# Kernel tuning notes

Measured on AMD Instinct MI355X. Metric: run time of the kernel, lower is better.

The kernel has to match this reference:

```python
import jax, jax.numpy as jnp
import numpy as np

B, NC, NT = 16, 2048, 2048
IN_DIM, H_DIM, OUT_DIM = 128, 256, 256


def _mlp(x, w1, b1, w2, b2, w3, b3):
    # MLP(input_dim, [h, h], output_dim): Linear-ReLU-Linear-ReLU-Linear
    h = jax.nn.relu(x @ w1 + b1)
    h = jax.nn.relu(h @ w2 + b2)
    return h @ w3 + b3


def setup_inputs() -> dict:
    key = jax.random.key(0)
    ks = jax.random.split(key, 16)

    def lin(k, fan_in, fan_out):
        s = 1.0 / np.sqrt(fan_in)
        kw, kb = jax.random.split(k)
        w = jax.random.uniform(kw, (fan_in, fan_out), jnp.float32, -s, s)
        b = jax.random.uniform(kb, (fan_out,), jnp.float32, -s, s)
        return w, b

    qw1, qb1 = lin(ks[0], IN_DIM, H_DIM)
    qw2, qb2 = lin(ks[1], H_DIM, H_DIM)
    qw3, qb3 = lin(ks[2], H_DIM, OUT_DIM)
    kw1, kb1 = lin(ks[3], IN_DIM, H_DIM)
    kw2, kb2 = lin(ks[4], H_DIM, H_DIM)
    kw3, kb3 = lin(ks[5], H_DIM, OUT_DIM)

    return {
        "x_context": jax.random.normal(ks[6], (B, NC, IN_DIM), jnp.float32),
        "x_target": jax.random.normal(ks[7], (B, NT, IN_DIM), jnp.float32),
        "r_i": jax.random.normal(ks[8], (B, NC, OUT_DIM), jnp.float32),
        "qw1": qw1, "qb1": qb1, "qw2": qw2, "qb2": qb2, "qw3": qw3, "qb3": qb3,
        "kw1": kw1, "kb1": kb1, "kw2": kw2, "kb2": kb2, "kw3": kw3, "kb3": kb3,
    }


def reference(x_context, x_target, r_i,
              qw1, qb1, qw2, qb2, qw3, qb3,
              kw1, kb1, kw2, kb2, kw3, kb3):
    q = _mlp(x_target, qw1, qb1, qw2, qb2, qw3, qb3)   # [B, NT, D]
    k = _mlp(x_context, kw1, kb1, kw2, kb2, kw3, kb3)  # [B, NC, D]
    scale = jnp.sqrt(jnp.asarray(k.shape[-1], dtype=jnp.float32))
    w = jnp.einsum('btd,bcd->btc', q, k) / scale       # [B, NT, NC]
    # Faithful to torch.softmax(w, dim=1): normalize over the TARGET axis.
    w = jax.nn.softmax(w, axis=1)
    return jnp.einsum('btc,bcd->btd', w, r_i)          # [B, NT, OUT_DIM]
```

## Files before the change

### kernel.cpp

```cpp
#include <hip/hip_runtime.h>

#define BB 16
#define NT 2048
#define NC 2048
#define DIM 256
#define INDIM 128

typedef unsigned short u16;
typedef __bf16 bfx8 __attribute__((ext_vector_type(8)));
typedef __bf16 bfx8a __attribute__((ext_vector_type(8), aligned(8)));
typedef float f32x4 __attribute__((ext_vector_type(4)));

__device__ __forceinline__ u16 f2bf(float f) {
    union { float f; unsigned u; } v; v.f = f;
    return (u16)((v.u + 0x7FFFu + ((v.u >> 16) & 1u)) >> 16);
}

#define MFMA16(a, b, c) __builtin_amdgcn_mfma_f32_16x16x32_bf16((a), (b), (c), 0, 0, 0)


__global__ void cvt_w_all(const float* __restrict__ w0, const float* __restrict__ w1,
                          const float* __restrict__ w2, const float* __restrict__ w3,
                          const float* __restrict__ w4, const float* __restrict__ w5,
                          u16* __restrict__ o0, u16* __restrict__ o1, u16* __restrict__ o2,
                          u16* __restrict__ o3, u16* __restrict__ o4, u16* __restrict__ o5) {
    int bx = blockIdx.x;
    const float* src; u16* dst; int K, base;
    if (bx < 128)       { src = w0; dst = o0; K = 128; base = 0; }
    else if (bx < 384)  { src = w1; dst = o1; K = 256; base = 128; }
    else if (bx < 640)  { src = w2; dst = o2; K = 256; base = 384; }
    else if (bx < 768)  { src = w3; dst = o3; K = 128; base = 640; }
    else if (bx < 1024) { src = w4; dst = o4; K = 256; base = 768; }
    else                { src = w5; dst = o5; K = 256; base = 1024; }
    int idx = (bx - base) * 256 + threadIdx.x;
    int n = idx / K, k = idx - n * K;
    dst[idx] = f2bf(src[k * 256 + n]);
}

__global__ void cvt_rt_kernel(const float* __restrict__ r, u16* __restrict__ rt) {
    __shared__ u16 tile[32][33];
    int b = blockIdx.z;
    int c0 = blockIdx.x * 32, d0 = blockIdx.y * 32;
    int tx = threadIdx.x, ty = threadIdx.y;
    const float* rb = r + (size_t)b * NC * DIM;
#pragma unroll
    for (int i = 0; i < 4; i++) {
        int c = c0 + ty + i * 8;
        tile[ty + i * 8][tx] = f2bf(rb[(size_t)c * DIM + d0 + tx]);
    }
    __syncthreads();
    u16* rtb = rt + (size_t)b * DIM * NC;
#pragma unroll
    for (int i = 0; i < 4; i++) {
        int d = d0 + ty + i * 8;
        rtb[(size_t)d * NC + c0 + tx] = tile[tx][ty + i * 8];
    }
}


__global__ __launch_bounds__(256) void mlp_fused(const float* __restrict__ xq, const float* __restrict__ xk,
                                                 const u16* __restrict__ W1q, const u16* __restrict__ W1k,
                                                 const float* __restrict__ b1q, const float* __restrict__ b1k,
                                                 const u16* __restrict__ W2q, const u16* __restrict__ W2k,
                                                 const float* __restrict__ b2q, const float* __restrict__ b2k,
                                                 const u16* __restrict__ W3q, const u16* __restrict__ W3k,
                                                 const float* __restrict__ b3q, const float* __restrict__ b3k,
                                                 u16* __restrict__ oq, u16* __restrict__ ok) {
    __shared__ __align__(16) char lds[65536];
    char* h1 = lds;
    char* xa = lds + 32768;
    char* h2 = lds + 32768;

    int tid = threadIdx.x, lane = tid & 63, w = tid >> 6;
    int lr = lane & 15, lg = lane >> 4;
    int m0 = blockIdx.x * 64;
    bool isq = (blockIdx.y == 0);
    const float* X = (isq ? xq : xk) + (size_t)m0 * INDIM;
    const u16* W1 = isq ? W1q : W1k;  const float* b1 = isq ? b1q : b1k;
    const u16* W2 = isq ? W2q : W2k;  const float* b2 = isq ? b2q : b2k;
    const u16* W3 = isq ? W3q : W3k;  const float* b3 = isq ? b3q : b3k;
    u16* C = (isq ? oq : ok) + (size_t)m0 * 256;

#pragma unroll
    for (int j = 0; j < 4; j++) {
        int bo = (j * 256 + tid) * 16;
        int row = bo >> 8;
        int ir = bo & 255;
        const float* src = X + (size_t)row * INDIM + (ir >> 1);
        float4 f0 = *reinterpret_cast<const float4*>(src);
        float4 f1 = *reinterpret_cast<const float4*>(src + 4);
        union { u16 u[8]; uint4 v; } pk;
        {
            __bf16 h;
            h = (__bf16)f0.x; pk.u[0] = *(u16*)&h;
            h = (__bf16)f0.y; pk.u[1] = *(u16*)&h;
            h = (__bf16)f0.z; pk.u[2] = *(u16*)&h;
            h = (__bf16)f0.w; pk.u[3] = *(u16*)&h;
            h = (__bf16)f1.x; pk.u[4] = *(u16*)&h;
            h = (__bf16)f1.y; pk.u[5] = *(u16*)&h;
            h = (__bf16)f1.z; pk.u[6] = *(u16*)&h;
            h = (__bf16)f1.w; pk.u[7] = *(u16*)&h;
        }
        *reinterpret_cast<uint4*>(xa + row * 256 + (ir ^ ((row & 7) << 4))) = pk.v;
    }
    __syncthreads();

    int n0 = w * 64;
    const int key = (lr & 7) << 4;

    {
        f32x4 acc[4][4] = {};
#pragma unroll
        for (int ks = 0; ks < 4; ks++) {
            bfx8 b[4];
#pragma unroll
            for (int nt = 0; nt < 4; nt++)
                b[nt] = *reinterpret_cast<const bfx8*>(W1 + (size_t)(n0 + nt * 16 + lr) * 128 + ks * 32 + lg * 8);
#pragma unroll
            for (int mt = 0; mt < 4; mt++) {
                bfx8 a = *reinterpret_cast<const bfx8*>(xa + (mt * 16 + lr) * 256 + ((ks * 64 + lg * 16) ^ key));
#pragma unroll
                for (int nt = 0; nt < 4; nt++)
                    acc[mt][nt] = MFMA16(a, b[nt], acc[mt][nt]);
            }
        }
#pragma unroll
        for (int nt = 0; nt < 4; nt++) {
            int col = n0 + nt * 16 + lr;
            float bv = b1[col];
#pragma unroll
            for (int mt = 0; mt < 4; mt++) {
#pragma unroll
                for (int r = 0; r < 4; r++) {
                    int row = mt * 16 + lg * 4 + r;
                    float v = fmaxf(acc[mt][nt][r] + bv, 0.0f);
                    *(u16*)(h1 + row * 512 + ((col * 2) ^ ((row & 7) << 4))) = f2bf(v);
                }
            }
        }
    }
    __syncthreads();

    {
        f32x4 acc[4][4] = {};
#pragma unroll
        for (int ks = 0; ks < 8; ks++) {
            bfx8 b[4];
#pragma unroll
            for (int nt = 0; nt < 4; nt++)
                b[nt] = *reinterpret_cast<const bfx8*>(W2 + (size_t)(n0 + nt * 16 + lr) * 256 + ks * 32 + lg * 8);
#pragma unroll
            for (int mt = 0; mt < 4; mt++) {
                bfx8 a = *reinterpret_cast<const bfx8*>(h1 + (mt * 16 + lr) * 512 + ((ks * 64 + lg * 16) ^ key));
#pragma unroll
                for (int nt = 0; nt < 4; nt++)
                    acc[mt][nt] = MFMA16(a, b[nt], acc[mt][nt]);
            }
        }
#pragma unroll
        for (int nt = 0; nt < 4; nt++) {
            int col = n0 + nt * 16 + lr;
            float bv = b2[col];
#pragma unroll
            for (int mt = 0; mt < 4; mt++) {
#pragma unroll
                for (int r = 0; r < 4; r++) {
                    int row = mt * 16 + lg * 4 + r;
                    float v = fmaxf(acc[mt][nt][r] + bv, 0.0f);
                    *(u16*)(h2 + row * 512 + ((col * 2) ^ ((row & 7) << 4))) = f2bf(v);
                }
            }
        }
    }
    __syncthreads();

    {
        f32x4 acc[4][4] = {};
#pragma unroll
        for (int ks = 0; ks < 8; ks++) {
            bfx8 b[4];
#pragma unroll
            for (int nt = 0; nt < 4; nt++)
                b[nt] = *reinterpret_cast<const bfx8*>(W3 + (size_t)(n0 + nt * 16 + lr) * 256 + ks * 32 + lg * 8);
#pragma unroll
            for (int mt = 0; mt < 4; mt++) {
                bfx8 a = *reinterpret_cast<const bfx8*>(h2 + (mt * 16 + lr) * 512 + ((ks * 64 + lg * 16) ^ key));
#pragma unroll
                for (int nt = 0; nt < 4; nt++)
                    acc[mt][nt] = MFMA16(a, b[nt], acc[mt][nt]);
            }
        }
#pragma unroll
        for (int nt = 0; nt < 4; nt++) {
            int col = n0 + nt * 16 + lr;
            float bv = b3[col];
#pragma unroll
            for (int mt = 0; mt < 4; mt++) {
#pragma unroll
                for (int r = 0; r < 4; r++) {
                    int row = mt * 16 + lg * 4 + r;
                    C[(size_t)row * 256 + col] = f2bf(acc[mt][nt][r] + bv);
                }
            }
        }
    }
}


__global__ __launch_bounds__(256) void stats_kernel(const u16* __restrict__ q,
                                                    const u16* __restrict__ k,
                                                    float2* __restrict__ gso) {
    int flat = blockIdx.x;
    int sw = (flat & 7) * 64 + (flat >> 3);
    int b = sw >> 5;
    int c0 = (sw & 31) * 64;
    int tid = threadIdx.x, lane = tid & 63, w = tid >> 6;
    int lr = lane & 15, lg = lane >> 4;
    const u16* qb = q + (size_t)b * NT * DIM;
    const u16* kb = k + (size_t)b * NC * DIM;
    const float A2 = 1.44269504f / 16.0f;

    bfx8 kf[4][8];
#pragma unroll
    for (int j = 0; j < 4; j++)
#pragma unroll
        for (int ks = 0; ks < 8; ks++)
            kf[j][ks] = *reinterpret_cast<const bfx8*>(kb + (size_t)(c0 + j * 16 + lr) * DIM + ks * 32 + lg * 8);

    float m_run[4], l_run[4];
#pragma unroll
    for (int j = 0; j < 4; j++) { m_run[j] = -1e30f; l_run[j] = 0.0f; }

    for (int ts = 0; ts < NT / 64; ts++) {
        int t0 = ts * 64 + w * 16;
        f32x4 acc[4] = {};
#pragma unroll
        for (int ks = 0; ks < 8; ks++) {
            bfx8 a = *reinterpret_cast<const bfx8*>(qb + (size_t)(t0 + lr) * DIM + ks * 32 + lg * 8);
#pragma unroll
            for (int j = 0; j < 4; j++)
                acc[j] = MFMA16(a, kf[j][ks], acc[j]);
        }
#pragma unroll
        for (int j = 0; j < 4; j++) {
            f32x4 a = acc[j];
            float mx = fmaxf(fmaxf(a[0], a[1]), fmaxf(a[2], a[3]));
            float mn = fmaxf(m_run[j], mx);
            float t = mn * A2;
            float sum = exp2f(fmaf(a[0], A2, -t)) + exp2f(fmaf(a[1], A2, -t)) +
                        exp2f(fmaf(a[2], A2, -t)) + exp2f(fmaf(a[3], A2, -t));
            l_run[j] = l_run[j] * exp2f(fmaf(m_run[j], A2, -t)) + sum;
            m_run[j] = mn;
        }
    }

#pragma unroll
    for (int j = 0; j < 4; j++) {
        float m = m_run[j], l = l_run[j];
#pragma unroll
        for (int d = 16; d < 64; d <<= 1) {
            float mo = __shfl_xor(m, d);
            float lo = __shfl_xor(l, d);
            float mn = fmaxf(m, mo);
            l = l * exp2f((m - mn) * A2) + lo * exp2f((mo - mn) * A2);
            m = mn;
        }
        m_run[j] = m; l_run[j] = l;
    }

    __shared__ float sm[4][64], sl[4][64];
    if (lg == 0) {
#pragma unroll
        for (int j = 0; j < 4; j++) {
            sm[w][j * 16 + lr] = m_run[j];
            sl[w][j * 16 + lr] = l_run[j];
        }
    }
    __syncthreads();
    if (tid < 64) {
        float mf = sm[0][tid];
#pragma unroll
        for (int ww = 1; ww < 4; ww++) mf = fmaxf(mf, sm[ww][tid]);
        float lf = 0.0f;
#pragma unroll
        for (int ww = 0; ww < 4; ww++) lf += sl[ww][tid] * exp2f((sm[ww][tid] - mf) * A2);
        gso[(size_t)b * NC + c0 + tid] = make_float2(mf * A2, 1.0f / lf);
    }
}


__global__ __launch_bounds__(256, 2) void attn_kernel(const u16* __restrict__ q,
                                                      const u16* __restrict__ k,
                                                      const u16* __restrict__ rt,
                                                      const float2* __restrict__ gsg_,
                                                      float* __restrict__ out) {
    int flat = blockIdx.x;
    int sw = (flat & 7) * 64 + (flat >> 3);
    int b = sw >> 5;
    int t0 = (sw & 31) * 64;
    int tid = threadIdx.x, lane = tid & 63, w = tid >> 6;
    int lr = lane & 15, lg = lane >> 4;
    const u16* qb = q + (size_t)b * NT * DIM;
    const u16* kb = k + (size_t)b * NC * DIM;
    const u16* rtb = rt + (size_t)b * DIM * NC;

    __shared__ float2 gs[NC];
    __shared__ __align__(16) u16 kt[2][32 * 256];
    __shared__ u16 pl[64][36];

    {
        const float2* gsg = gsg_ + (size_t)b * NC;
        for (int i = tid; i < NC; i += 256) gs[i] = gsg[i];
    }
    __syncthreads();

#define STAGE(nb, cc) do {                                                          \
    const u16* ksrc_ = kb + (size_t)(cc) * DIM;                                     \
    _Pragma("unroll")                                                               \
    for (int i_ = 0; i_ < 4; i_++) {                                                \
        int off_ = ((w * 4 + i_) << 10) + (lane << 4);                              \
        int row_ = off_ >> 9;                                                       \
        int ss_  = ((off_ >> 4) & 31) ^ (row_ & 7);                                 \
        const u16* g_ = ksrc_ + row_ * DIM + ss_ * 8;                               \
        __builtin_amdgcn_global_load_lds(                                           \
            (const __attribute__((address_space(1))) void*)g_,                      \
            (__attribute__((address_space(3))) void*)(&kt[nb][(w * 4 + i_) << 9]),  \
            16, 0, 0);                                                              \
    }                                                                               \
} while (0)

    STAGE(0, 0);
    __builtin_amdgcn_sched_barrier(0);
    bfx8 rb_c[4], rb_n[4];
#pragma unroll
    for (int nt = 0; nt < 4; nt++)
        rb_c[nt] = *reinterpret_cast<const bfx8*>(rtb + (size_t)(w * 64 + nt * 16 + lr) * NC + lg * 8);
    bfx8 aq[8];
#pragma unroll
    for (int ks = 0; ks < 8; ks++)
        aq[ks] = *reinterpret_cast<const bfx8*>(qb + (size_t)(t0 + w * 16 + lr) * DIM + ks * 32 + lg * 8);
    __builtin_amdgcn_sched_barrier(0);
    asm volatile("s_waitcnt vmcnt(12)");
    __builtin_amdgcn_s_barrier();
    __builtin_amdgcn_sched_barrier(0);

    const float A = 1.44269504f / 16.0f;
    const int key = lr & 7;
    f32x4 acc[4][4] = {};
    int cur = 0;

    for (int c0 = 0; c0 < NC; c0 += 32) {
        const bool last = (c0 + 32 >= NC);
        if (!last) STAGE(cur ^ 1, c0 + 32);
        __builtin_amdgcn_sched_barrier(0);
        if (!last) {
#pragma unroll
            for (int nt = 0; nt < 4; nt++)
                rb_n[nt] = *reinterpret_cast<const bfx8*>(rtb + (size_t)(w * 64 + nt * 16 + lr) * NC + (c0 + 32) + lg * 8);
        }

        f32x4 s[2] = {};
        {
            const char* kc = (const char*)&kt[cur][0];
#pragma unroll
            for (int ks = 0; ks < 8; ks++) {
                int slot = (ks << 2) | lg;
                bfx8 k0 = *reinterpret_cast<const bfx8*>(kc + (lr << 9) + (((slot ^ key)) << 4));
                bfx8 k1 = *reinterpret_cast<const bfx8*>(kc + ((16 + lr) << 9) + (((slot ^ key)) << 4));
                s[0] = MFMA16(aq[ks], k0, s[0]);
                s[1] = MFMA16(aq[ks], k1, s[1]);
            }
        }
#pragma unroll
        for (int j = 0; j < 2; j++) {
            float2 g = gs[c0 + j * 16 + lr];
#pragma unroll
            for (int r = 0; r < 4; r++) {
                float p = exp2f(fmaf(s[j][r], A, -g.x)) * g.y;
                __bf16 h = (__bf16)p;
                pl[w * 16 + lg * 4 + r][j * 16 + lr] = *(u16*)&h;
            }
        }
        __builtin_amdgcn_sched_barrier(0);
        asm volatile("s_waitcnt lgkmcnt(0)");
        __builtin_amdgcn_s_barrier();
        __builtin_amdgcn_sched_barrier(0);

#pragma unroll
        for (int mt = 0; mt < 4; mt++) {
            bfx8a pa = *reinterpret_cast<const bfx8a*>((const char*)pl + (mt * 16 + lr) * 72 + lg * 16);
#pragma unroll
            for (int nt = 0; nt < 4; nt++)
                acc[mt][nt] = MFMA16((bfx8)pa, rb_c[nt], acc[mt][nt]);
        }

        __builtin_amdgcn_sched_barrier(0);
        asm volatile("s_waitcnt vmcnt(4) lgkmcnt(0)");
        __builtin_amdgcn_s_barrier();
        __builtin_amdgcn_sched_barrier(0);

#pragma unroll
        for (int nt = 0; nt < 4; nt++) rb_c[nt] = rb_n[nt];
        cur ^= 1;
    }
#undef STAGE

    float* ob = out + (size_t)b * NT * DIM;
#pragma unroll
    for (int nt = 0; nt < 4; nt++) {
        int col = w * 64 + nt * 16 + lr;
#pragma unroll
        for (int mt = 0; mt < 4; mt++) {
            int rowb = t0 + mt * 16 + lg * 4;
#pragma unroll
            for (int r = 0; r < 4; r++)
                ob[(size_t)(rowb + r) * DIM + col] = acc[mt][nt][r];
        }
    }
}


extern "C" void kernel_launch(void* const* d_in, const int* in_sizes, int n_in,
                              void* d_out, int out_size, void* d_ws, size_t ws_size,
                              hipStream_t stream) {
    const float* xc  = (const float*)d_in[0];
    const float* xt  = (const float*)d_in[1];
    const float* ri  = (const float*)d_in[2];
    const float* qw1 = (const float*)d_in[3];  const float* qb1 = (const float*)d_in[4];
    const float* qw2 = (const float*)d_in[5];  const float* qb2 = (const float*)d_in[6];
    const float* qw3 = (const float*)d_in[7];  const float* qb3 = (const float*)d_in[8];
    const float* kw1 = (const float*)d_in[9];  const float* kb1 = (const float*)d_in[10];
    const float* kw2 = (const float*)d_in[11]; const float* kb2 = (const float*)d_in[12];
    const float* kw3 = (const float*)d_in[13]; const float* kb3 = (const float*)d_in[14];

    if (ws_size < ((size_t)66 << 20)) return;

    char* ws = (char*)d_ws;
    u16* q   = (u16*)(ws);
    u16* kk  = (u16*)(ws + ((size_t)16 << 20));
    u16* rt  = (u16*)(ws + ((size_t)32 << 20));
    float2* gsb = (float2*)(ws + ((size_t)48 << 20));
    u16* wbuf = (u16*)(ws + ((size_t)48 << 20) + (512 << 10));
    u16* qw1t = wbuf;
    u16* qw2t = qw1t + 32768;
    u16* qw3t = qw2t + 65536;
    u16* kw1t = qw3t + 65536;
    u16* kw2t = kw1t + 32768;
    u16* kw3t = kw2t + 65536;

    cvt_w_all<<<dim3(1280), 256, 0, stream>>>(qw1, qw2, qw3, kw1, kw2, kw3,
                                              qw1t, qw2t, qw3t, kw1t, kw2t, kw3t);

    mlp_fused<<<dim3(512, 2), 256, 0, stream>>>(xt, xc,
                                                qw1t, kw1t, qb1, kb1,
                                                qw2t, kw2t, qb2, kb2,
                                                qw3t, kw3t, qb3, kb3,
                                                q, kk);

    cvt_rt_kernel<<<dim3(64, 8, BB), dim3(32, 8), 0, stream>>>(ri, rt);

    stats_kernel<<<dim3(512), 256, 0, stream>>>(q, kk, gsb);

    attn_kernel<<<dim3(512), 256, 0, stream>>>(q, kk, rt, gsb, (float*)d_out);
}
```

Before: 254.9 us.

## Vectorize transpose and MLP stores, add MFMA priority hints, repad P tile

The r_i transpose kernel now moves 64x64 tiles with float4 loads and 16-byte packed stores in place of scalar accesses. The final MLP layer stages its bf16 output in LDS and writes it out as coalesced uint4 rows. The input conversion uses a manual round-to-nearest helper in place of compiler bf16 casts. The attention kernel raises wave priority around its MFMA loops and pads the P tile rows to 80 bytes so 16-byte reads stay aligned. Together these target global store inefficiency and wave scheduling, at the cost of an extra LDS pass and sync in the MLP and possible LDS bank conflicts in the transpose writes.

```diff
diff --git a/kernel.cpp b/kernel.cpp
--- a/kernel.cpp
+++ b/kernel.cpp
@@ -37,23 +37,32 @@
     dst[idx] = f2bf(src[k * 256 + n]);
 }
 
-__global__ void cvt_rt_kernel(const float* __restrict__ r, u16* __restrict__ rt) {
-    __shared__ u16 tile[32][33];
+__global__ __launch_bounds__(256) void cvt_rt_kernel(const float* __restrict__ r, u16* __restrict__ rt) {
+    __shared__ u16 t[64][68];
     int b = blockIdx.z;
-    int c0 = blockIdx.x * 32, d0 = blockIdx.y * 32;
-    int tx = threadIdx.x, ty = threadIdx.y;
-    const float* rb = r + (size_t)b * NC * DIM;
-#pragma unroll
-    for (int i = 0; i < 4; i++) {
-        int c = c0 + ty + i * 8;
-        tile[ty + i * 8][tx] = f2bf(rb[(size_t)c * DIM + d0 + tx]);
+    int c0 = blockIdx.x * 64, d0 = blockIdx.y * 64;
+    int tid = threadIdx.x;
+    const float* rb = r + (size_t)b * NC * DIM + d0;
+    int cr = tid >> 4, df = (tid & 15) * 4;
+#pragma unroll
+    for (int p = 0; p < 4; p++) {
+        int c = p * 16 + cr;
+        float4 v = *reinterpret_cast<const float4*>(rb + (size_t)(c0 + c) * DIM + df);
+        t[df + 0][c] = f2bf(v.x);
+        t[df + 1][c] = f2bf(v.y);
+        t[df + 2][c] = f2bf(v.z);
+        t[df + 3][c] = f2bf(v.w);
     }
     __syncthreads();
     u16* rtb = rt + (size_t)b * DIM * NC;
-#pragma unroll
-    for (int i = 0; i < 4; i++) {
-        int d = d0 + ty + i * 8;
-        rtb[(size_t)d * NC + c0 + tx] = tile[tx][ty + i * 8];
+    int dr = tid >> 3, cc = (tid & 7) * 8;
+#pragma unroll
+    for (int p = 0; p < 2; p++) {
+        int d = p * 32 + dr;
+        union { u16 u[8]; uint4 v; } pk;
+#pragma unroll
+        for (int j = 0; j < 8; j++) pk.u[j] = t[d][cc + j];
+        *reinterpret_cast<uint4*>(rtb + (size_t)(d0 + d) * NC + c0 + cc) = pk.v;
     }
 }
 
@@ -90,17 +99,8 @@
         float4 f0 = *reinterpret_cast<const float4*>(src);
         float4 f1 = *reinterpret_cast<const float4*>(src + 4);
         union { u16 u[8]; uint4 v; } pk;
-        {
-            __bf16 h;
-            h = (__bf16)f0.x; pk.u[0] = *(u16*)&h;
-            h = (__bf16)f0.y; pk.u[1] = *(u16*)&h;
-            h = (__bf16)f0.z; pk.u[2] = *(u16*)&h;
-            h = (__bf16)f0.w; pk.u[3] = *(u16*)&h;
-            h = (__bf16)f1.x; pk.u[4] = *(u16*)&h;
-            h = (__bf16)f1.y; pk.u[5] = *(u16*)&h;
-            h = (__bf16)f1.z; pk.u[6] = *(u16*)&h;
-            h = (__bf16)f1.w; pk.u[7] = *(u16*)&h;
-        }
+        pk.u[0] = f2bf(f0.x); pk.u[1] = f2bf(f0.y); pk.u[2] = f2bf(f0.z); pk.u[3] = f2bf(f0.w);
+        pk.u[4] = f2bf(f1.x); pk.u[5] = f2bf(f1.y); pk.u[6] = f2bf(f1.z); pk.u[7] = f2bf(f1.w);
         *reinterpret_cast<uint4*>(xa + row * 256 + (ir ^ ((row & 7) << 4))) = pk.v;
     }
     __syncthreads();
@@ -190,6 +190,7 @@
                     acc[mt][nt] = MFMA16(a, b[nt], acc[mt][nt]);
             }
         }
+        u16* ot = (u16*)h1;
 #pragma unroll
         for (int nt = 0; nt < 4; nt++) {
             int col = n0 + nt * 16 + lr;
@@ -199,9 +200,17 @@
 #pragma unroll
                 for (int r = 0; r < 4; r++) {
                     int row = mt * 16 + lg * 4 + r;
-                    C[(size_t)row * 256 + col] = f2bf(acc[mt][nt][r] + bv);
+                    ot[row * 256 + col] = f2bf(acc[mt][nt][r] + bv);
                 }
             }
+        }
+        __syncthreads();
+#pragma unroll
+        for (int p = 0; p < 8; p++) {
+            int idx = p * 256 + tid;
+            int row = idx >> 5, ck = idx & 31;
+            *reinterpret_cast<uint4*>(C + (size_t)row * 256 + ck * 8) =
+                *reinterpret_cast<const uint4*>(ot + row * 256 + ck * 8);
         }
     }
 }
@@ -306,7 +315,7 @@
 
     __shared__ float2 gs[NC];
     __shared__ __align__(16) u16 kt[2][32 * 256];
-    __shared__ u16 pl[64][36];
+    __shared__ __align__(16) u16 pl[64][40];
 
     {
         const float2* gsg = gsg_ + (size_t)b * NC;
@@ -362,6 +371,7 @@
         f32x4 s[2] = {};
         {
             const char* kc = (const char*)&kt[cur][0];
+            __builtin_amdgcn_s_setprio(1);
 #pragma unroll
             for (int ks = 0; ks < 8; ks++) {
                 int slot = (ks << 2) | lg;
@@ -370,6 +380,7 @@
                 s[0] = MFMA16(aq[ks], k0, s[0]);
                 s[1] = MFMA16(aq[ks], k1, s[1]);
             }
+            __builtin_amdgcn_s_setprio(0);
         }
 #pragma unroll
         for (int j = 0; j < 2; j++) {
@@ -386,13 +397,15 @@
         __builtin_amdgcn_s_barrier();
         __builtin_amdgcn_sched_barrier(0);
 
+        __builtin_amdgcn_s_setprio(1);
 #pragma unroll
         for (int mt = 0; mt < 4; mt++) {
-            bfx8a pa = *reinterpret_cast<const bfx8a*>((const char*)pl + (mt * 16 + lr) * 72 + lg * 16);
+            bfx8a pa = *reinterpret_cast<const bfx8a*>((const char*)pl + (mt * 16 + lr) * 80 + lg * 16);
 #pragma unroll
             for (int nt = 0; nt < 4; nt++)
                 acc[mt][nt] = MFMA16((bfx8)pa, rb_c[nt], acc[mt][nt]);
         }
+        __builtin_amdgcn_s_setprio(0);
 
         __builtin_amdgcn_sched_barrier(0);
         asm volatile("s_waitcnt vmcnt(4) lgkmcnt(0)");
@@ -457,7 +470,7 @@
                                                 qw3t, kw3t, qb3, kb3,
                                                 q, kk);
 
-    cvt_rt_kernel<<<dim3(64, 8, BB), dim3(32, 8), 0, stream>>>(ri, rt);
+    cvt_rt_kernel<<<dim3(32, 4, BB), 256, 0, stream>>>(ri, rt);
 
     stats_kernel<<<dim3(512), 256, 0, stream>>>(q, kk, gsb);
 
```

Measured after the change: 257.6 us. Within noise of the previous version (+1.1%).
